# Kernel tuning notes

Hardware: AMD Instinct MI355X
Metric: run time of the kernel (lower is better)

Reference implementation:

```python
import jax, jax.numpy as jnp
import numpy as np

THRESHOLD = 0.5
NEG_POS_RATIO = 3
ALPHA = 1.0


def cxcy_to_xy(c):
    # (cx,cy,w,h) -> (xmin,ymin,xmax,ymax)
    return jnp.concatenate([c[..., :2] - c[..., 2:] / 2.0,
                            c[..., :2] + c[..., 2:] / 2.0], axis=-1)


def gcxgcy_to_cxcy(g, priors):
    # standard SSD decode with variances (10, 5)
    return jnp.concatenate([g[..., :2] * priors[..., 2:] / 10.0 + priors[..., :2],
                            jnp.exp(g[..., 2:] / 5.0) * priors[..., 2:]], axis=-1)


def jaccard(set1, set2):
    # set1: [n1,4], set2: [n2,4], xyxy -> IoU matrix [n1,n2]
    lo = jnp.maximum(set1[:, None, :2], set2[None, :, :2])
    hi = jnp.minimum(set1[:, None, 2:], set2[None, :, 2:])
    wh = jnp.clip(hi - lo, 0.0)
    inter = wh[..., 0] * wh[..., 1]
    a1 = (set1[:, 2] - set1[:, 0]) * (set1[:, 3] - set1[:, 1])
    a2 = (set2[:, 2] - set2[:, 0]) * (set2[:, 3] - set2[:, 1])
    return inter / (a1[:, None] + a2[None, :] - inter)


def match_one(b, l, priors_xy):
    # b: [n_obj,4] GT boxes, l: [n_obj] labels, priors_xy: [P,4]
    n_obj = b.shape[0]
    ov = jaccard(b, priors_xy)                      # [n_obj, P]
    obj_for_prior = jnp.argmax(ov, axis=0)          # [P]
    ov_for_prior = jnp.max(ov, axis=0)              # [P]
    prior_for_obj = jnp.argmax(ov, axis=1)          # [n_obj]
    # force each object to own its best prior
    obj_for_prior = obj_for_prior.at[prior_for_obj].set(jnp.arange(n_obj))
    ov_for_prior = ov_for_prior.at[prior_for_obj].set(1.0)
    lab = l[obj_for_prior]
    lab = jnp.where(ov_for_prior < THRESHOLD, 0, lab)
    return lab, b[obj_for_prior]


def ciou(b1, b2):
    # elementwise CIoU over [..., 4] xyxy boxes -> [...]
    w1 = b1[..., 2] - b1[..., 0]; h1 = b1[..., 3] - b1[..., 1]
    w2 = b2[..., 2] - b2[..., 0]; h2 = b2[..., 3] - b2[..., 1]
    area1 = w1 * h1; area2 = w2 * h2
    cx1 = (b1[..., 2] + b1[..., 0]) / 2; cy1 = (b1[..., 3] + b1[..., 1]) / 2
    cx2 = (b2[..., 2] + b2[..., 0]) / 2; cy2 = (b2[..., 3] + b2[..., 1]) / 2
    in_wh = jnp.clip(jnp.minimum(b1[..., 2:], b2[..., 2:]) - jnp.maximum(b1[..., :2], b2[..., :2]), 0.0)
    out_wh = jnp.clip(jnp.maximum(b1[..., 2:], b2[..., 2:]) - jnp.minimum(b1[..., :2], b2[..., :2]), 0.0)
    inner_diag = (cx2 - cx1) ** 2 + (cy2 - cy1) ** 2
    outer_diag = out_wh[..., 0] ** 2 + out_wh[..., 1] ** 2
    inner = in_wh[..., 0] * in_wh[..., 1]
    iou = inner / (area1 + area2 - inner)
    v = (4.0 / (np.pi ** 2)) * (jnp.arctan(w2 / h2) - jnp.arctan(w1 / h1)) ** 2
    alpha = jax.lax.stop_gradient(v / (1.0 - iou + v))  # torch.no_grad()
    return 1.0 - iou + inner_diag / outer_diag + alpha * v


def setup_inputs() -> dict:
    key = jax.random.key(0)
    ks = jax.random.split(key, 7)
    N, P, C, NOBJ = 32, 8732, 81, 24
    predicted_locs = jax.random.normal(ks[0], (N, P, 4), jnp.float32)
    predicted_scores = jax.random.normal(ks[1], (N, P, C), jnp.float32)
    mins = jax.random.uniform(ks[2], (N, NOBJ, 2), minval=0.0, maxval=0.7)
    sizes = jax.random.uniform(ks[3], (N, NOBJ, 2), minval=0.05, maxval=0.3)
    boxes = jnp.concatenate([mins, mins + sizes], axis=-1)  # well-formed xyxy
    labels = jax.random.randint(ks[4], (N, NOBJ), 1, C)      # 1..C-1 (0 = background)
    pc = jax.random.uniform(ks[5], (P, 2), minval=0.05, maxval=0.95)
    pwh = jax.random.uniform(ks[6], (P, 2), minval=0.05, maxval=0.5)
    priors_cxcy = jnp.concatenate([pc, pwh], axis=-1)
    return {"predicted_locs": predicted_locs, "predicted_scores": predicted_scores,
            "boxes": boxes, "labels": labels, "priors_cxcy": priors_cxcy}


def reference(predicted_locs, predicted_scores, boxes, labels, priors_cxcy):
    priors_xy = cxcy_to_xy(priors_cxcy)
    # per-image GT->prior matching (vectorized over batch)
    true_classes, decoded_true = jax.vmap(match_one, in_axes=(0, 0, None))(boxes, labels, priors_xy)
    decoded_pred = cxcy_to_xy(gcxgcy_to_cxcy(predicted_locs, priors_cxcy[None]))  # [N,P,4]
    pos = true_classes != 0                              # [N,P]
    posf = pos.astype(predicted_locs.dtype)
    n_pos_total = jnp.sum(posf)
    # localization: CIoU mean over positive priors
    loc_loss = jnp.sum(ciou(decoded_pred, decoded_true) * posf) / n_pos_total
    # confidence: CE per prior
    logp = jax.nn.log_softmax(predicted_scores, axis=-1)
    conf_all = -jnp.take_along_axis(logp, true_classes[..., None], axis=-1)[..., 0]  # [N,P]
    conf_pos_sum = jnp.sum(conf_all * posf)
    # hard negative mining: top (neg_pos_ratio * n_pos) negatives per image
    conf_neg = jnp.where(pos, 0.0, conf_all)
    conf_neg_sorted = -jnp.sort(-conf_neg, axis=1)       # descending
    n_hard = NEG_POS_RATIO * jnp.sum(pos, axis=1)        # [N]
    ranks = jnp.arange(conf_neg_sorted.shape[1])[None, :]
    hard_mask = (ranks < n_hard[:, None]).astype(conf_all.dtype)
    conf_hard_neg_sum = jnp.sum(conf_neg_sorted * hard_mask)
    conf_loss = (conf_hard_neg_sum + conf_pos_sum) / n_pos_total
    return conf_loss + ALPHA * loc_loss
```

## Files before the change

kernel.cpp:

```cpp
#include <hip/hip_runtime.h>
#include <math.h>

#define BLK  256
#define BLKM 1024

constexpr int N_IMG = 32;
constexpr int P_PRI = 8732;
constexpr int C_CLS = 81;
constexpr int N_OBJ = 24;
constexpr int RPB   = 112;
constexpr int PB2   = (P_PRI + RPB - 1) / RPB;
constexpr int NBLK2 = PB2 * N_IMG;
constexpr int LROW  = 84;
constexpr int NLD   = 9;

__global__ void k_obj_match(const float* __restrict__ boxes,
                            const float* __restrict__ priors,
                            int* __restrict__ prior_for_obj,
                            int* __restrict__ npos) {
    const int o = blockIdx.x;
    const int n = blockIdx.y;
    const int tid = threadIdx.x;

    if (o == 0 && tid == 0) npos[n] = 0;

    const float x1 = boxes[(n * N_OBJ + o) * 4 + 0];
    const float y1 = boxes[(n * N_OBJ + o) * 4 + 1];
    const float x2 = boxes[(n * N_OBJ + o) * 4 + 2];
    const float y2 = boxes[(n * N_OBJ + o) * 4 + 3];
    const float ab = (x2 - x1) * (y2 - y1);

    const float4* pr4 = (const float4*)priors;

    float bv = -1.0f;
    int   bi = P_PRI;
    for (int p = tid; p < P_PRI; p += BLK) {
        const float4 c = pr4[p];
        const float px1 = c.x - c.z / 2.0f, py1 = c.y - c.w / 2.0f;
        const float px2 = c.x + c.z / 2.0f, py2 = c.y + c.w / 2.0f;
        const float pa  = (px2 - px1) * (py2 - py1);
        const float lox = fmaxf(x1, px1), loy = fmaxf(y1, py1);
        const float hix = fminf(x2, px2), hiy = fminf(y2, py2);
        const float iw = fmaxf(hix - lox, 0.0f), ih = fmaxf(hiy - loy, 0.0f);
        const float inter = iw * ih;
        const float iou = inter / (ab + pa - inter);
        if (iou > bv) { bv = iou; bi = p; }
    }

    __shared__ float sv[BLK];
    __shared__ int   si[BLK];
    sv[tid] = bv; si[tid] = bi;
    __syncthreads();
    for (int s = BLK / 2; s > 0; s >>= 1) {
        if (tid < s) {
            const float v2 = sv[tid + s]; const int i2 = si[tid + s];
            if (v2 > sv[tid] || (v2 == sv[tid] && i2 < si[tid])) { sv[tid] = v2; si[tid] = i2; }
        }
        __syncthreads();
    }
    if (tid == 0) prior_for_obj[n * N_OBJ + o] = si[0];
}

__global__ void __launch_bounds__(BLK, 4)
k_main(const float* __restrict__ locs,
       const float* __restrict__ scores,
       const float* __restrict__ boxes,
       const int*   __restrict__ labels,
       const float* __restrict__ priors,
       const int*   __restrict__ prior_for_obj,
       float* __restrict__ conf_neg,
       int*   __restrict__ npos,
       float* __restrict__ partial_conf,
       float* __restrict__ partial_loc) {
    __shared__ float sdata[RPB * LROW];
    __shared__ int   pfo[N_OBJ];
    __shared__ float wred[4][4];

    const int n   = blockIdx.y;
    const int r0  = blockIdx.x * RPB;
    const int tid = threadIdx.x;
    const int rows = min(RPB, P_PRI - r0);
    const int nvec = (rows * C_CLS) >> 2;

    const float4* src = (const float4*)(scores + ((size_t)n * P_PRI + r0) * C_CLS);
    float4 ld[NLD];
#pragma unroll
    for (int k = 0; k < NLD; ++k) {
        const int i = tid + k * BLK;
        if (i < nvec) ld[k] = src[i];
    }

    if (tid < N_OBJ) pfo[tid] = prior_for_obj[n * N_OBJ + tid];

    const int row = tid >> 1;
    const int h   = tid & 1;
    const int p   = r0 + row;
    const int psafe = (p < P_PRI) ? p : (P_PRI - 1);
    const float4 c = ((const float4*)priors)[psafe];
    const float px1 = c.x - c.z / 2.0f, py1 = c.y - c.w / 2.0f;
    const float px2 = c.x + c.z / 2.0f, py2 = c.y + c.w / 2.0f;
    const float pa  = (px2 - px1) * (py2 - py1);

    float bestv = -1.0f;
    int   besto = 0;
    const float4* bxg = (const float4*)(boxes + (size_t)n * N_OBJ * 4);
#pragma unroll
    for (int o = 0; o < N_OBJ; ++o) {
        const float4 b = bxg[o];
        const float lox = fmaxf(b.x, px1), loy = fmaxf(b.y, py1);
        const float hix = fminf(b.z, px2), hiy = fminf(b.w, py2);
        const float iw = fmaxf(hix - lox, 0.0f), ih = fmaxf(hiy - loy, 0.0f);
        const float inter = iw * ih;
        const float ab = (b.z - b.x) * (b.w - b.y);
        const float iou = inter / (ab + pa - inter);
        if (iou > bestv) { bestv = iou; besto = o; }
    }

#pragma unroll
    for (int k = 0; k < NLD; ++k) {
        const int i = tid + k * BLK;
        if (i < nvec) {
            const int f  = i * 4;
            const int r  = (int)((unsigned)f / 81u);
            const int cc = f - r * 81;
            const int base = r * LROW + cc;
            const float vv[4] = {ld[k].x, ld[k].y, ld[k].z, ld[k].w};
#pragma unroll
            for (int j = 0; j < 4; ++j) {
                int a = base + j;
                if (cc + j >= 81) a += (LROW - C_CLS);
                sdata[a] = vv[j];
            }
        }
    }
    __syncthreads();

    int   obj = besto;
    float ov  = bestv;
#pragma unroll
    for (int o = 0; o < N_OBJ; ++o)
        if (pfo[o] == p) { obj = o; ov = 1.0f; }

    float s = 0.0f;
    const float* rbase = sdata + row * LROW;
    if (row < rows) {
        const float4* rv = (const float4*)(rbase + 40 * h);
#pragma unroll
        for (int q = 0; q < 10; ++q) {
            const float4 v = rv[q];
            s += __expf(v.x) + __expf(v.y) + __expf(v.z) + __expf(v.w);
        }
        if (h) s += __expf(rbase[80]);
    }
    s += __shfl_xor(s, 1);

    int cls = labels[n * N_OBJ + obj];
    if (ov < 0.5f) cls = 0;

    float confpos = 0.0f, locv = 0.0f;
    int   cnt1 = 0;
    if (h == 0 && row < rows) {
        const float conf = __logf(s) - rbase[cls];
        const bool pos = (cls != 0);
        conf_neg[n * P_PRI + p] = pos ? 0.0f : fmaxf(conf, 0.0f);
        if (pos) {
            cnt1 = 1;
            confpos = conf;
            const float4 g = ((const float4*)locs)[(size_t)n * P_PRI + p];
            const float cx = g.x * c.z / 10.0f + c.x;
            const float cy = g.y * c.w / 10.0f + c.y;
            const float w  = expf(g.z / 5.0f) * c.z;
            const float hh = expf(g.w / 5.0f) * c.w;
            const float b1x1 = cx - w / 2.0f, b1y1 = cy - hh / 2.0f;
            const float b1x2 = cx + w / 2.0f, b1y2 = cy + hh / 2.0f;

            const float4 tb = bxg[obj];
            const float w1 = b1x2 - b1x1, h1 = b1y2 - b1y1;
            const float w2 = tb.z - tb.x, h2 = tb.w - tb.y;
            const float area1 = w1 * h1,  area2 = w2 * h2;
            const float c1x = (b1x2 + b1x1) / 2.0f, c1y = (b1y2 + b1y1) / 2.0f;
            const float c2x = (tb.z + tb.x) / 2.0f, c2y = (tb.w + tb.y) / 2.0f;
            const float inw = fmaxf(fminf(b1x2, tb.z) - fmaxf(b1x1, tb.x), 0.0f);
            const float inh = fmaxf(fminf(b1y2, tb.w) - fmaxf(b1y1, tb.y), 0.0f);
            const float owd = fmaxf(fmaxf(b1x2, tb.z) - fminf(b1x1, tb.x), 0.0f);
            const float ohd = fmaxf(fmaxf(b1y2, tb.w) - fminf(b1y1, tb.y), 0.0f);
            const float inner_diag = (c2x - c1x) * (c2x - c1x) + (c2y - c1y) * (c2y - c1y);
            const float outer_diag = owd * owd + ohd * ohd;
            const float inner = inw * inh;
            const float iou = inner / (area1 + area2 - inner);
            const float K = 0.40528473456935108577551785283891f;
            const float dat = atanf(w2 / h2) - atanf(w1 / h1);
            const float v = K * dat * dat;
            const float alpha = v / (1.0f - iou + v);
            locv = 1.0f - iou + inner_diag / outer_diag + alpha * v;
        }
    }

#pragma unroll
    for (int off = 32; off > 0; off >>= 1) {
        confpos += __shfl_down(confpos, off);
        locv    += __shfl_down(locv, off);
        cnt1    += __shfl_down(cnt1, off);
    }
    const int wid = tid >> 6;
    if ((tid & 63) == 0) {
        wred[wid][0] = confpos; wred[wid][1] = locv; wred[wid][2] = (float)cnt1;
    }
    __syncthreads();
    if (tid == 0) {
        float a = 0.0f, b = 0.0f, d = 0.0f;
#pragma unroll
        for (int w2 = 0; w2 < 4; ++w2) { a += wred[w2][0]; b += wred[w2][1]; d += wred[w2][2]; }
        const int slot = n * gridDim.x + blockIdx.x;
        partial_conf[slot] = a;
        partial_loc [slot] = b;
        atomicAdd(&npos[n], (int)d);
    }
}

__global__ void __launch_bounds__(BLKM)
k_mine(const float* __restrict__ conf_neg,
       const int*   __restrict__ npos,
       float* __restrict__ hardneg) {
    __shared__ int   wcnt[2][BLKM / 64];
    __shared__ float wsum[BLKM / 64];

    const int n    = blockIdx.x;
    const int tid  = threadIdx.x;
    const int wid  = tid >> 6;
    const int lane = tid & 63;

    unsigned v[9];
#pragma unroll
    for (int k = 0; k < 9; ++k) {
        const int p = tid + k * BLKM;
        v[k] = (p < P_PRI) ? __float_as_uint(conf_neg[n * P_PRI + p]) : 0u;
    }

    int k0 = 3 * npos[n];
    if (k0 > P_PRI) k0 = P_PRI;
    if (k0 <= 0) { if (tid == 0) hardneg[n] = 0.0f; return; }

    unsigned prefix = 0u;
    int kk = k0;
    for (int bit = 30; bit >= 0; --bit) {
        const unsigned hi = (prefix >> bit) | 1u;
        int cnt = 0;
#pragma unroll
        for (int k = 0; k < 9; ++k)
            cnt += __popcll(__ballot((v[k] >> bit) == hi));
        if (lane == 0) wcnt[bit & 1][wid] = cnt;
        __syncthreads();
        int tot = 0;
#pragma unroll
        for (int w = 0; w < BLKM / 64; ++w) tot += wcnt[bit & 1][w];
        if (tot >= kk) prefix |= (1u << bit);
        else           kk -= tot;
    }

    float psum = 0.0f; int pcnt = 0;
#pragma unroll
    for (int k = 0; k < 9; ++k) {
        if (v[k] > prefix) { psum += __uint_as_float(v[k]); ++pcnt; }
    }
#pragma unroll
    for (int off = 32; off > 0; off >>= 1) {
        psum += __shfl_down(psum, off);
        pcnt += __shfl_down(pcnt, off);
    }
    __syncthreads();
    if (lane == 0) { wsum[wid] = psum; wcnt[0][wid] = pcnt; }
    __syncthreads();
    if (tid == 0) {
        float S = 0.0f; int C = 0;
#pragma unroll
        for (int w = 0; w < BLKM / 64; ++w) { S += wsum[w]; C += wcnt[0][w]; }
        hardneg[n] = S + (float)(k0 - C) * __uint_as_float(prefix);
    }
}

__global__ void k_final(const float* __restrict__ partial_conf,
                        const float* __restrict__ partial_loc,
                        const int*   __restrict__ npos,
                        const float* __restrict__ hardneg,
                        float* __restrict__ out) {
    __shared__ float s1[BLK], s2[BLK], s3[BLK];
    __shared__ int   si[BLK];
    const int tid = threadIdx.x;

    float c = 0.0f, l = 0.0f, h = 0.0f;
    int np = 0;
    for (int i = tid; i < NBLK2; i += BLK) { c += partial_conf[i]; l += partial_loc[i]; }
    if (tid < N_IMG) { h = hardneg[tid]; np = npos[tid]; }

    s1[tid] = c; s2[tid] = l; s3[tid] = h; si[tid] = np;
    __syncthreads();
    for (int s = BLK / 2; s > 0; s >>= 1) {
        if (tid < s) { s1[tid] += s1[tid + s]; s2[tid] += s2[tid + s];
                       s3[tid] += s3[tid + s]; si[tid] += si[tid + s]; }
        __syncthreads();
    }
    if (tid == 0) {
        const float npt = (float)si[0];
        const float conf_loss = (s3[0] + s1[0]) / npt;
        const float loc_loss  = s2[0] / npt;
        out[0] = conf_loss + loc_loss;
    }
}

extern "C" void kernel_launch(void* const* d_in, const int* in_sizes, int n_in,
                              void* d_out, int out_size, void* d_ws, size_t ws_size,
                              hipStream_t stream) {
    const float* locs   = (const float*)d_in[0];
    const float* scores = (const float*)d_in[1];
    const float* boxes  = (const float*)d_in[2];
    const int*   labels = (const int*)  d_in[3];
    const float* priors = (const float*)d_in[4];
    float* out = (float*)d_out;

    char* w = (char*)d_ws;
    float* conf_neg      = (float*)w; w += (size_t)N_IMG * P_PRI * 4;
    int*   prior_for_obj = (int*)w;   w += (size_t)N_IMG * N_OBJ * 4;
    int*   npos          = (int*)w;   w += (size_t)N_IMG * 4;
    float* partial_conf  = (float*)w; w += (size_t)NBLK2 * 4;
    float* partial_loc   = (float*)w; w += (size_t)NBLK2 * 4;
    float* hardneg       = (float*)w; w += (size_t)N_IMG * 4;

    dim3 gridO(N_OBJ, N_IMG);
    k_obj_match<<<gridO, BLK, 0, stream>>>(boxes, priors, prior_for_obj, npos);

    dim3 gridM(PB2, N_IMG);
    k_main<<<gridM, BLK, 0, stream>>>(locs, scores, boxes, labels, priors,
                                      prior_for_obj, conf_neg, npos,
                                      partial_conf, partial_loc);

    k_mine<<<N_IMG, BLKM, 0, stream>>>(conf_neg, npos, hardneg);

    k_final<<<1, BLK, 0, stream>>>(partial_conf, partial_loc, npos, hardneg, out);
}
```

Baseline: 78.69 us.

## Use four threads per prior row with smaller blocks and shuffle-reduced matching

Reduces rows per block from 112 to 64 and assigns four threads per prior instead of two. Each thread now handles a quarter of the IoU matching against the ground-truth objects and a quarter of the softmax exp-sum, and the partial results are combined with warp shuffles. Labels are staged in shared memory, and the launch bound is raised to allow more resident blocks. The intent is to increase parallelism and occupancy. The cost is more blocks to schedule and extra shuffle work per row.

Result: slower. 88.44 us (+12.4%).

```diff
diff --git a/kernel.cpp b/kernel.cpp
--- a/kernel.cpp
+++ b/kernel.cpp
@@ -8,11 +8,11 @@
 constexpr int P_PRI = 8732;
 constexpr int C_CLS = 81;
 constexpr int N_OBJ = 24;
-constexpr int RPB   = 112;
+constexpr int RPB   = 64;
 constexpr int PB2   = (P_PRI + RPB - 1) / RPB;
 constexpr int NBLK2 = PB2 * N_IMG;
 constexpr int LROW  = 84;
-constexpr int NLD   = 9;
+constexpr int NLD   = 6;
 
 __global__ void k_obj_match(const float* __restrict__ boxes,
                             const float* __restrict__ priors,
@@ -61,7 +61,7 @@
     if (tid == 0) prior_for_obj[n * N_OBJ + o] = si[0];
 }
 
-__global__ void __launch_bounds__(BLK, 4)
+__global__ void __launch_bounds__(BLK, 7)
 k_main(const float* __restrict__ locs,
        const float* __restrict__ scores,
        const float* __restrict__ boxes,
@@ -74,6 +74,7 @@
        float* __restrict__ partial_loc) {
     __shared__ float sdata[RPB * LROW];
     __shared__ int   pfo[N_OBJ];
+    __shared__ int   slab[N_OBJ];
     __shared__ float wred[4][4];
 
     const int n   = blockIdx.y;
@@ -91,9 +92,10 @@
     }
 
     if (tid < N_OBJ) pfo[tid] = prior_for_obj[n * N_OBJ + tid];
-
-    const int row = tid >> 1;
-    const int h   = tid & 1;
+    if (tid >= 64 && tid < 64 + N_OBJ) slab[tid - 64] = labels[n * N_OBJ + (tid - 64)];
+
+    const int row = tid >> 2;
+    const int q   = tid & 3;
     const int p   = r0 + row;
     const int psafe = (p < P_PRI) ? p : (P_PRI - 1);
     const float4 c = ((const float4*)priors)[psafe];
@@ -101,11 +103,12 @@
     const float px2 = c.x + c.z / 2.0f, py2 = c.y + c.w / 2.0f;
     const float pa  = (px2 - px1) * (py2 - py1);
 
-    float bestv = -1.0f;
-    int   besto = 0;
     const float4* bxg = (const float4*)(boxes + (size_t)n * N_OBJ * 4);
-#pragma unroll
-    for (int o = 0; o < N_OBJ; ++o) {
+    float bv = -1.0f;
+    int   bo = q * 6;
+#pragma unroll
+    for (int j = 0; j < 6; ++j) {
+        const int o = q * 6 + j;
         const float4 b = bxg[o];
         const float lox = fmaxf(b.x, px1), loy = fmaxf(b.y, py1);
         const float hix = fminf(b.z, px2), hiy = fminf(b.w, py2);
@@ -113,7 +116,13 @@
         const float inter = iw * ih;
         const float ab = (b.z - b.x) * (b.w - b.y);
         const float iou = inter / (ab + pa - inter);
-        if (iou > bestv) { bestv = iou; besto = o; }
+        if (iou > bv) { bv = iou; bo = o; }
+    }
+#pragma unroll
+    for (int m = 1; m < 4; m <<= 1) {
+        const float v2 = __shfl_xor(bv, m);
+        const int   o2 = __shfl_xor(bo, m);
+        if (v2 > bv || (v2 == bv && o2 < bo)) { bv = v2; bo = o2; }
     }
 
 #pragma unroll
@@ -135,31 +144,41 @@
     }
     __syncthreads();
 
-    int   obj = besto;
-    float ov  = bestv;
-#pragma unroll
-    for (int o = 0; o < N_OBJ; ++o)
-        if (pfo[o] == p) { obj = o; ov = 1.0f; }
+    int fo = -1;
+#pragma unroll
+    for (int j = 0; j < 6; ++j) {
+        const int o = q * 6 + j;
+        if (pfo[o] == p) fo = o;
+    }
+#pragma unroll
+    for (int m = 1; m < 4; m <<= 1) fo = max(fo, __shfl_xor(fo, m));
+
+    int   obj = (fo >= 0) ? fo : bo;
+    float ov  = (fo >= 0) ? 1.0f : bv;
 
     float s = 0.0f;
     const float* rbase = sdata + row * LROW;
     if (row < rows) {
-        const float4* rv = (const float4*)(rbase + 40 * h);
-#pragma unroll
-        for (int q = 0; q < 10; ++q) {
-            const float4 v = rv[q];
-            s += __expf(v.x) + __expf(v.y) + __expf(v.z) + __expf(v.w);
+        const float4* rv = (const float4*)(rbase + 20 * q);
+        float a0 = 0.0f, a1 = 0.0f;
+#pragma unroll
+        for (int i = 0; i < 5; ++i) {
+            const float4 v = rv[i];
+            a0 += __expf(v.x) + __expf(v.y);
+            a1 += __expf(v.z) + __expf(v.w);
         }
-        if (h) s += __expf(rbase[80]);
+        s = a0 + a1;
+        if (q == 3) s += __expf(rbase[80]);
     }
     s += __shfl_xor(s, 1);
-
-    int cls = labels[n * N_OBJ + obj];
+    s += __shfl_xor(s, 2);
+
+    int cls = slab[obj];
     if (ov < 0.5f) cls = 0;
 
     float confpos = 0.0f, locv = 0.0f;
     int   cnt1 = 0;
-    if (h == 0 && row < rows) {
+    if (q == 0 && row < rows) {
         const float conf = __logf(s) - rbase[cls];
         const bool pos = (cls != 0);
         conf_neg[n * P_PRI + p] = pos ? 0.0f : fmaxf(conf, 0.0f);
```
